# Optimization experiments

Measured on AMD Instinct MI355X. Metric: run time of the kernel, lower is better.

The kernel has to match this reference:

```python
import jax, jax.numpy as jnp
import numpy as np

B, C, T, H, W = 1, 512, 8, 48, 48
GROUPS = 32
EPS = 1e-6


def setup_inputs() -> dict:
    key = jax.random.key(0)
    ks = jax.random.split(key, 6)
    s = 0.02  # init scale for projection weights
    return {
        "x": jax.random.normal(ks[0], (B, C, T, H, W), dtype=jnp.float32),
        "gamma": jnp.ones((C,), dtype=jnp.float32),
        "beta": jnp.zeros((C,), dtype=jnp.float32),
        "wq": jax.random.normal(ks[1], (C, C), dtype=jnp.float32) * s,
        "bq": jnp.zeros((C,), dtype=jnp.float32),
        "wk": jax.random.normal(ks[2], (C, C), dtype=jnp.float32) * s,
        "bk": jnp.zeros((C,), dtype=jnp.float32),
        "wv": jax.random.normal(ks[3], (C, C), dtype=jnp.float32) * s,
        "bv": jnp.zeros((C,), dtype=jnp.float32),
        "wo": jax.random.normal(ks[4], (C, C), dtype=jnp.float32) * s,
        "bo": jnp.zeros((C,), dtype=jnp.float32),
    }


def _group_norm(x, gamma, beta):
    b, c, t, h, w = x.shape
    xg = x.reshape(b, GROUPS, c // GROUPS, t, h, w)
    mu = xg.mean(axis=(2, 3, 4, 5), keepdims=True)
    var = xg.var(axis=(2, 3, 4, 5), keepdims=True)
    xn = ((xg - mu) * jax.lax.rsqrt(var + EPS)).reshape(b, c, t, h, w)
    return xn * gamma[None, :, None, None, None] + beta[None, :, None, None, None]


def _proj(h, wgt, bias):
    # CausalConv3d with kernel_size=1 == pointwise channel linear
    return jnp.einsum('oc,bcthw->bothw', wgt, h) + bias[None, :, None, None, None]


def reference(x, gamma, beta, wq, bq, wk, bk, wv, bv, wo, bo):
    hn = _group_norm(x, gamma, beta)
    q = _proj(hn, wq, bq)
    k = _proj(hn, wk, bk)
    v = _proj(hn, wv, bv)
    b, c, t, h, w = q.shape
    n = h * w
    # per-frame spatial attention: (b, t, n, c)
    qf = q.transpose(0, 2, 3, 4, 1).reshape(b, t, n, c)
    kf = k.transpose(0, 2, 3, 4, 1).reshape(b, t, n, c)
    vf = v.transpose(0, 2, 3, 4, 1).reshape(b, t, n, c)
    scores = jnp.einsum('btqc,btkc->btqk', qf, kf) * (c ** -0.5)
    attn = jax.nn.softmax(scores, axis=-1)
    of = jnp.einsum('btqk,btkc->btqc', attn, vf)
    o = of.reshape(b, t, h, w, c).transpose(0, 4, 1, 2, 3)
    o = _proj(o, wo, bo)
    return x + o
```

## Files before the change

### kernel.cpp

```cpp
#include <hip/hip_runtime.h>
#include <hip/hip_bf16.h>
#include <cstdint>
#include <type_traits>

typedef __attribute__((ext_vector_type(8))) __bf16 bf16x8;
typedef __attribute__((ext_vector_type(4))) float f32x4;
typedef __attribute__((ext_vector_type(2))) long longx2;

struct bf2frag { bf16x8 k0, k1; };

__device__ __forceinline__ float bf2f(unsigned short u) {
  union { uint32_t i; float f; } v; v.i = (uint32_t)u << 16; return v.f;
}
__device__ __forceinline__ unsigned short f2bf(float f) {
  union { float f; uint32_t i; } v{f};
  uint32_t r = v.i + 0x7fffu + ((v.i >> 16) & 1u);
  return (unsigned short)(r >> 16);
}

__device__ __forceinline__ void gll(const void* g, void* l) {
  __builtin_amdgcn_global_load_lds(
      (const __attribute__((address_space(1))) uint32_t*)(uintptr_t)g,
      (__attribute__((address_space(3))) uint32_t*)(uint32_t)(uintptr_t)l,
      16, 0, 0);
}

__device__ __forceinline__ void bar() {
  asm volatile("" ::: "memory");
  __builtin_amdgcn_s_barrier();
  asm volatile("" ::: "memory");
}

#define VMCNT(n) asm volatile("s_waitcnt vmcnt(" #n ")" ::: "memory")

template <int N>
__device__ __forceinline__ void vmw() {
  if constexpr (N == 0) { VMCNT(0); }
  else if constexpr (N == 1) { VMCNT(1); }
  else if constexpr (N == 2) { VMCNT(2); }
  else if constexpr (N == 3) { VMCNT(3); }
  else if constexpr (N == 4) { VMCNT(4); }
  else if constexpr (N == 5) { VMCNT(5); }
  else if constexpr (N == 6) { VMCNT(6); }
  else if constexpr (N == 7) { VMCNT(7); }
  else if constexpr (N == 8) { VMCNT(8); }
  else if constexpr (N == 9) { VMCNT(9); }
  else if constexpr (N == 10) { VMCNT(10); }
  else { VMCNT(12); }
}

__device__ __forceinline__ f32x4 mma(bf16x8 a, bf16x8 b, f32x4 c) {
  return __builtin_amdgcn_mfma_f32_16x16x32_bf16(a, b, c, 0, 0, 0);
}
__device__ __forceinline__ f32x4 mma(long a, long b, f32x4 c) {
  return __builtin_amdgcn_mfma_f32_16x16x32_fp8_fp8(a, b, c, 0, 0, 0);
}
__device__ __forceinline__ f32x4 mmak(const bf2frag& a, const bf2frag& b, f32x4 c, int k2) {
  return k2 ? mma(a.k1, b.k1, c) : mma(a.k0, b.k0, c);
}
__device__ __forceinline__ f32x4 mmak(longx2 a, longx2 b, f32x4 c, int k2) {
  return mma(a[k2], b[k2], c);
}

__device__ __forceinline__ int perm64(int m) {
  return (m & ~63) | (((m >> 3) & 3) << 4) | (((m >> 5) & 1) << 3) | (m & 7);
}

__global__ __launch_bounds__(256) void stats_partial_k(const float* __restrict__ x,
                                                       float* __restrict__ part) {
  const int g = blockIdx.x >> 3, p = blockIdx.x & 7;
  const float* base = x + (long)g * 16 * 18432 + (long)p * 2304;
  float s = 0.f, ss = 0.f;
  for (int idx = threadIdx.x; idx < 16 * 576; idx += 256) {
    const int c = idx / 576, i4 = idx % 576;
    const float4 v = *(const float4*)(base + (long)c * 18432 + i4 * 4);
    s += v.x + v.y + v.z + v.w;
    ss += v.x * v.x + v.y * v.y + v.z * v.z + v.w * v.w;
  }
  __shared__ float rs[256], rss[256];
  rs[threadIdx.x] = s; rss[threadIdx.x] = ss;
  __syncthreads();
  for (int o = 128; o > 0; o >>= 1) {
    if ((int)threadIdx.x < o) { rs[threadIdx.x] += rs[threadIdx.x + o]; rss[threadIdx.x] += rss[threadIdx.x + o]; }
    __syncthreads();
  }
  if (threadIdx.x == 0) { part[blockIdx.x * 2] = rs[0]; part[blockIdx.x * 2 + 1] = rss[0]; }
}

__global__ void stats_final_k(const float* __restrict__ part, float* __restrict__ stats) {
  const int g = threadIdx.x;
  if (g < 32) {
    float s = 0.f, ss = 0.f;
    for (int p = 0; p < 8; ++p) { s += part[(g * 8 + p) * 2]; ss += part[(g * 8 + p) * 2 + 1]; }
    const float mean = s / 294912.0f;
    const float var = ss / 294912.0f - mean * mean;
    stats[g * 2] = mean;
    stats[g * 2 + 1] = rsqrtf(var + 1e-6f);
  }
}

__global__ __launch_bounds__(256) void gn_transpose_k(const float* __restrict__ x,
                                                      const float* __restrict__ stats,
                                                      const float* __restrict__ gamma,
                                                      const float* __restrict__ beta,
                                                      unsigned short* __restrict__ hnT) {
  __shared__ float tile[64][65];
  const int c0 = blockIdx.x * 64, n0 = blockIdx.y * 64;
  const int tn = threadIdx.x & 63, tr = threadIdx.x >> 6;
  for (int cc = tr; cc < 64; cc += 4) {
    const int c = c0 + cc, g = c >> 4;
    const float mean = stats[g * 2], rstd = stats[g * 2 + 1];
    const float v = x[(long)c * 18432 + n0 + tn];
    tile[cc][tn] = (v - mean) * rstd * gamma[c] + beta[c];
  }
  __syncthreads();
  for (int nn = tr; nn < 64; nn += 4) {
    hnT[(long)(n0 + nn) * 512 + c0 + tn] = f2bf(tile[tn][nn]);
  }
}

__global__ __launch_bounds__(256) void pack_bf16_k(const float* __restrict__ w,
                                                   unsigned short* __restrict__ o) {
  const int i = (blockIdx.x * 256 + threadIdx.x) * 4;
  const float4 v = *(const float4*)(w + i);
  ushort4 u; u.x = f2bf(v.x); u.y = f2bf(v.y); u.z = f2bf(v.z); u.w = f2bf(v.w);
  *(ushort4*)(o + i) = u;
}

__global__ void pack_bias_k(const float* __restrict__ bq, const float* __restrict__ bk,
                            float* __restrict__ bqk) {
  const int t = threadIdx.x;
  bqk[t] = (t < 512) ? bq[t] : bk[t - 512];
}

__global__ __launch_bounds__(256) void combine_k(const float* __restrict__ rs,
                                                 float* __restrict__ linv, int ntile) {
  const int row = blockIdx.x * 256 + threadIdx.x;
  const int t = row / 2304, r = row % 2304;
  float L = 0.f;
  for (int x = 0; x < ntile; ++x) L += rs[((long)(t * ntile + x)) * 2304 + r];
  linv[row] = 1.0f / L;
}

template <int BM, int BIAS_MODE, int OUT_MODE, int STATS, int SCALEN, int MODE, int FP8, int P2,
          int WL = 0>
__global__ __launch_bounds__((BM == 256) ? 512 : 256, (WL && FP8) ? 4 : 2)
void gemm256(const void* __restrict__ A, long lda, long sAz,
             const void* __restrict__ B, long ldb, long sBz,
             void* __restrict__ Cp, long ldc, long sCz,
             const float* __restrict__ bias,
             const float* __restrict__ resid,
             float* __restrict__ rowsums,
             const float* __restrict__ linv,
             float alpha, int K, int gx, int gy) {
  constexpr int EB = FP8 ? 1 : 2;
  constexpr int THREADS = (BM == 256) ? 512 : 256;
  constexpr int BN = WL ? 128 : 256;
  constexpr int HBA = (BM / 2) * 64 * EB;
  constexpr int HBB = (BN / 2) * 64 * EB;
  constexpr int GA = HBA / (THREADS * 16);
  constexpr int GB = HBB / (THREADS * 16);
  constexpr int V0 = GB + 2 * GA, V3 = 2 * GB + GA, VP = GB + GA;
  constexpr int NSLOT = WL ? 8 : ((BM == 256) ? 8 : 4);
  constexpr int NSLOTP = NSLOT + 1;
  constexpr int MR = WL ? 4 : 8;
  constexpr int FQ = WL ? 2 : 4;
  constexpr int PRIO = !P2;
  __shared__ alignas(16) unsigned char As[2][2][HBA];
  __shared__ alignas(16) unsigned char Bs[2][2][HBB];
  using ABt2 = typename std::conditional<FP8, longx2, bf2frag>::type;

  const int tid = threadIdx.x;
  const int lane = tid & 63, wid = tid >> 6;
  const int wm = WL ? (wid >> 1) : ((BM == 256) ? (wid & 1) : 0);
  const int wn = WL ? (wid & 1) : ((BM == 256) ? (wid >> 1) : wid);
  int bx, by, bz;
  {
    const int g8 = blockIdx.x & 7, n = blockIdx.x >> 3;
    if (MODE == 0) { bz = g8; bx = n % gx; by = n / gx; }
    else if (MODE == 1) { bz = 0; bx = n % gx; by = g8 * gy + n / gx; }
    else { bz = 0; by = n % gy; bx = g8 * gx + n / gy; }
  }
  const unsigned char* Ab = (const unsigned char*)A + ((long)bz * sAz + (long)bx * BM * lda) * EB;
  const unsigned char* Bb = (const unsigned char*)B + ((long)bz * sBz + (long)by * BN * ldb) * EB;

  auto stageA = [&](int slot, int h, int k0) {
    if constexpr (!FP8) {
      const int ksw = ((tid & 7) << 3) ^ (((tid >> 3) & 7) << 3);
#pragma unroll
      for (int call = 0; call < GA; ++call) {
        const int r = call * (THREADS / 8) + (tid >> 3);
        const int grow = WL ? (((r >> 5) << 6) + h * 32 + (r & 31))
                            : (((r >> 6) << 7) + h * 64 + (r & 63));
        gll(Ab + ((long)grow * lda + k0) * 2 + ksw * 2, &As[slot][h][call * THREADS * 16 + tid * 16]);
      }
    } else {
#pragma unroll
      for (int call = 0; call < GA; ++call) {
        const int l = call * (THREADS / 4) + (tid >> 2);
        const int grow = WL ? (((l >> 5) << 6) + h * 32 + (l & 31))
                            : (((l >> 6) << 7) + h * 64 + (l & 63));
        const int x = (((l & 3) ^ ((l >> 2) & 3)) << 4);
        gll(Ab + (long)grow * lda + k0 + (((tid & 3) << 4) ^ x),
            &As[slot][h][call * THREADS * 16 + tid * 16]);
      }
    }
  };
  auto stageB = [&](int slot, int h, int k0) {
    if constexpr (!FP8) {
      const int ksw = ((tid & 7) << 3) ^ (((tid >> 3) & 7) << 3);
#pragma unroll
      for (int call = 0; call < GB; ++call) {
        const int r = call * (THREADS / 8) + (tid >> 3);
        const int grow = ((r >> 5) << 6) + h * 32 + (r & 31);
        gll(Bb + ((long)grow * ldb + k0) * 2 + ksw * 2, &Bs[slot][h][call * THREADS * 16 + tid * 16]);
      }
    } else {
#pragma unroll
      for (int call = 0; call < GB; ++call) {
        const int l = call * (THREADS / 4) + (tid >> 2);
        const int grow = ((l >> 5) << 6) + h * 32 + (l & 31);
        const int x = (((l & 3) ^ ((l >> 2) & 3)) << 4);
        gll(Bb + (long)grow * ldb + k0 + (((tid & 3) << 4) ^ x),
            &Bs[slot][h][call * THREADS * 16 + tid * 16]);
      }
    }
  };
  auto ldA = [&](int slot, int mh, int fq) -> ABt2 {
    const int r = (WL ? wm * 32 : wm * 64) + fq * 16 + (lane & 15);
    if constexpr (!FP8) {
      bf2frag f;
      const int kk0 = (((lane >> 4) << 3)) ^ ((r & 7) << 3);
      const int kk1 = (32 + ((lane >> 4) << 3)) ^ ((r & 7) << 3);
      f.k0 = *reinterpret_cast<const bf16x8*>(&As[slot][mh][r * 128 + kk0 * 2]);
      f.k1 = *reinterpret_cast<const bf16x8*>(&As[slot][mh][r * 128 + kk1 * 2]);
      return f;
    } else {
      const int x = (((r & 3) ^ ((r >> 2) & 3)) << 4);
      const int kk = ((lane >> 4) << 4) ^ x;
      return *reinterpret_cast<const longx2*>(&As[slot][mh][r * 64 + kk]);
    }
  };
  auto ldB = [&](int slot, int nh, int g) -> ABt2 {
    const int r = wn * 32 + g * 16 + (lane & 15);
    if constexpr (!FP8) {
      bf2frag f;
      const int kk0 = (((lane >> 4) << 3)) ^ ((r & 7) << 3);
      const int kk1 = (32 + ((lane >> 4) << 3)) ^ ((r & 7) << 3);
      f.k0 = *reinterpret_cast<const bf16x8*>(&Bs[slot][nh][r * 128 + kk0 * 2]);
      f.k1 = *reinterpret_cast<const bf16x8*>(&Bs[slot][nh][r * 128 + kk1 * 2]);
      return f;
    } else {
      const int x = (((r & 3) ^ ((r >> 2) & 3)) << 4);
      const int kk = ((lane >> 4) << 4) ^ x;
      return *reinterpret_cast<const longx2*>(&Bs[slot][nh][r * 64 + kk]);
    }
  };

  f32x4 acc[MR][4] = {};
  ABt2 a[4], b0[2], b1[2];

#define READ_A(SLOT, MH)                                                     \
  _Pragma("unroll") for (int fq = 0; fq < FQ; ++fq) a[fq] = ldA(SLOT, MH, fq);
#define READ_B(SLOT, NH, DST)                                                \
  _Pragma("unroll") for (int g = 0; g < 2; ++g) DST[g] = ldB(SLOT, NH, g);
#define MFMA_QUAD(MH, NH, BARR)                                              \
  if constexpr (PRIO) __builtin_amdgcn_s_setprio(1);                         \
  _Pragma("unroll") for (int fq = 0; fq < FQ; ++fq)                          \
    _Pragma("unroll") for (int g = 0; g < 2; ++g)                            \
      _Pragma("unroll") for (int k2 = 0; k2 < 2; ++k2)                       \
        acc[(MH) * FQ + fq][(NH) * 2 + g] =                                  \
            mmak(a[fq], BARR[g], acc[(MH) * FQ + fq][(NH) * 2 + g], k2);     \
  if constexpr (PRIO) __builtin_amdgcn_s_setprio(0);

  const int KT = K >> 6;
  stageB(0, 0, 0);
  stageA(0, 0, 0);
  stageB(0, 1, 0);
  stageA(0, 1, 0);
  stageB(1, 0, 64);
  if constexpr (!P2) stageA(1, 1, 64);
  vmw<VP>();
  bar();

  if constexpr (!P2) {
    for (int W = 0; W < KT; ++W) {
      const int s = W & 1;
      const int kn1 = (W + 1) << 6, kn2 = (W + 2) << 6;
      const bool st1 = (W + 1 < KT), st2 = (W + 2 < KT);
      READ_A(s, 0)
      READ_B(s, 0, b0)
      if (st1) stageA(s ^ 1, 0, kn1);
      bar();
      MFMA_QUAD(0, 0, b0)
      if (st1) { vmw<V0>(); }
      bar();
      READ_B(s, 1, b1)
      if (st1) stageB(s ^ 1, 1, kn1);
      bar();
      MFMA_QUAD(0, 1, b1)
      bar();
      READ_A(s, 1)
      if (st2) stageB(s, 0, kn2);
      bar();
      MFMA_QUAD(1, 1, b1)
      bar();
      if (st2) stageA(s, 1, kn2);
      bar();
      MFMA_QUAD(1, 0, b0)
      if (st2) { vmw<V3>(); } else { vmw<0>(); }
      bar();
    }
  } else {
    for (int W = 0; W < KT; ++W) {
      const int s = W & 1;
      const int kn1 = (W + 1) << 6, kn2 = (W + 2) << 6;
      const bool st1 = (W + 1 < KT), st2 = (W + 2 < KT);
      READ_A(s, 0)
      READ_B(s, 0, b0)
      READ_B(s, 1, b1)
      if (st1) { stageA(s ^ 1, 0, kn1); stageB(s ^ 1, 1, kn1); stageA(s ^ 1, 1, kn1); }
      bar();
      MFMA_QUAD(0, 0, b0)
      MFMA_QUAD(0, 1, b1)
      if (st1) { vmw<2 * (GA + GB)>(); } else { vmw<0>(); }
      bar();
      READ_A(s, 1)
      if (st2) stageB(s, 0, kn2);
      bar();
      MFMA_QUAD(1, 1, b1)
      MFMA_QUAD(1, 0, b0)
      if (st2) { vmw<GA + GB>(); } else if (st1) { vmw<GA>(); } else { vmw<0>(); }
      bar();
    }
  }

  const int mg0 = bx * BM + (WL ? wm * 64 : wm * 128) + ((lane >> 4) << 2);
  const int ng0 = by * BN + wn * 64 + (lane & 15);
  float* red = (float*)&As[0][0][0];
#pragma unroll
  for (int N = 0; N < 4; ++N) {
    const int n = ng0 + (N >> 1) * 32 + (N & 1) * 16;
    const float bn = (BIAS_MODE == 2) ? bias[n] : 0.f;
    const float sc = SCALEN ? linv[(long)bz * 2304 + n] : 1.0f;
    float eN = 0.f;
#pragma unroll
    for (int M = 0; M < MR; ++M) {
      const int m = mg0 + (WL ? ((M >> 1) * 32 + (M & 1) * 16) : ((M >> 2) * 64 + (M & 3) * 16));
      const f32x4 av = acc[M][N];
      float vals[4];
#pragma unroll
      for (int j = 0; j < 4; ++j) {
        vals[j] = av[j] * alpha + ((BIAS_MODE == 1) ? bias[m + j] : bn);
        if (SCALEN) vals[j] *= sc;
        if (STATS) { vals[j] = __expf(vals[j]); eN += vals[j]; }
      }
      if (OUT_MODE == 0) {
        ushort4 o; o.x = f2bf(vals[0]); o.y = f2bf(vals[1]); o.z = f2bf(vals[2]); o.w = f2bf(vals[3]);
        *(ushort4*)((unsigned short*)Cp + (long)bz * sCz + (long)n * ldc + m) = o;
      } else if (OUT_MODE == 2) {
        int pk = __builtin_amdgcn_cvt_pk_fp8_f32(vals[0], vals[1], 0, false);
        pk = __builtin_amdgcn_cvt_pk_fp8_f32(vals[2], vals[3], pk, true);
        *(int*)((unsigned char*)Cp + (long)bz * sCz + (long)n * ldc + perm64(m)) = pk;
      } else {
        const float* rp = resid + (long)n * ldc + m;
        float4 o; o.x = vals[0] + rp[0]; o.y = vals[1] + rp[1]; o.z = vals[2] + rp[2]; o.w = vals[3] + rp[3];
        *(float4*)((float*)Cp + (long)bz * sCz + (long)n * ldc + m) = o;
      }
    }
    if (STATS) {
      const int nloc = wn * 64 + (N >> 1) * 32 + (N & 1) * 16 + (lane & 15);
      const int slot = wm * 4 + (lane >> 4);
      red[nloc * NSLOTP + slot] = eN;
    }
  }
  if (STATS) {
    bar();
    if (tid < BN) {
      float L = 0.f;
#pragma unroll
      for (int s2 = 0; s2 < NSLOT; ++s2) L += red[tid * NSLOTP + s2];
      rowsums[((long)(bz * gx + bx)) * 2304 + by * BN + tid] = L;
    }
  }
#undef READ_A
#undef READ_B
#undef MFMA_QUAD
}

extern "C" void kernel_launch(void* const* d_in, const int* in_sizes, int n_in,
                              void* d_out, int out_size, void* d_ws, size_t ws_size,
                              hipStream_t stream) {
  const float* x = (const float*)d_in[0];
  const float* gamma = (const float*)d_in[1];
  const float* beta = (const float*)d_in[2];
  const float* wq = (const float*)d_in[3];
  const float* bq = (const float*)d_in[4];
  const float* wk = (const float*)d_in[5];
  const float* bk = (const float*)d_in[6];
  const float* wv = (const float*)d_in[7];
  const float* bv = (const float*)d_in[8];
  const float* wo = (const float*)d_in[9];
  const float* bo = (const float*)d_in[10];
  float* out = (float*)d_out;

  char* ws = (char*)d_ws;
  size_t off = 0;
  auto alloc = [&](size_t bytes) {
    char* p = ws + off;
    off = (off + bytes + 255) & ~(size_t)255;
    return p;
  };
  float* part = (float*)alloc(256 * 2 * sizeof(float));
  float* stats = (float*)alloc(32 * 2 * sizeof(float));
  unsigned short* wqkb = (unsigned short*)alloc((size_t)2 * 262144 * 2);
  unsigned short* wvb = (unsigned short*)alloc((size_t)262144 * 2);
  unsigned short* wob = (unsigned short*)alloc((size_t)262144 * 2);
  float* bqk = (float*)alloc(1024 * sizeof(float));
  float* rowsums = (float*)alloc((size_t)8 * 18 * 2304 * sizeof(float));
  float* linv = (float*)alloc((size_t)18432 * sizeof(float));
  unsigned short* hnT = (unsigned short*)alloc((size_t)18432 * 512 * 2);
  unsigned char* qkA = (unsigned char*)alloc((size_t)18432 * 1024);
  unsigned char* vT = (unsigned char*)alloc((size_t)512 * 18432);
  unsigned char* Sm = (unsigned char*)alloc((size_t)8 * 2304 * 2304);
  unsigned short* Ob = hnT;
  (void)ws_size; (void)in_sizes; (void)n_in; (void)out_size;

  stats_partial_k<<<dim3(256), dim3(256), 0, stream>>>(x, part);
  stats_final_k<<<dim3(1), dim3(64), 0, stream>>>(part, stats);
  gn_transpose_k<<<dim3(8, 288), dim3(256), 0, stream>>>(x, stats, gamma, beta, hnT);
  pack_bf16_k<<<dim3(256), dim3(256), 0, stream>>>(wq, wqkb);
  pack_bf16_k<<<dim3(256), dim3(256), 0, stream>>>(wk, wqkb + 262144);
  pack_bf16_k<<<dim3(256), dim3(256), 0, stream>>>(wv, wvb);
  pack_bf16_k<<<dim3(256), dim3(256), 0, stream>>>(wo, wob);
  pack_bias_k<<<dim3(1), dim3(1024), 0, stream>>>(bq, bk, bqk);

  gemm256<128, 1, 2, 0, 0, 1, 0, 1, 1><<<dim3(1152), dim3(256), 0, stream>>>(
      wqkb, 512, 0, hnT, 512, 0, (void*)qkA, 1024, 0, bqk, nullptr, nullptr, nullptr,
      1.0f, 512, 8, 18);
  gemm256<128, 2, 2, 0, 0, 2, 0, 1, 1><<<dim3(576), dim3(256), 0, stream>>>(
      hnT, 512, 0, wvb, 512, 0, (void*)vT, 18432, 0, bv, nullptr, nullptr, nullptr,
      1.0f, 512, 18, 4);
  gemm256<128, 0, 2, 1, 0, 0, 1, 1, 1><<<dim3(2592), dim3(256), 0, stream>>>(
      qkA + 512, 1024, (long)2304 * 1024, qkA, 1024, (long)2304 * 1024, (void*)Sm, 2304,
      (long)2304 * 2304, nullptr, nullptr, rowsums, nullptr,
      0.044194173824159216f, 512, 18, 18);
  combine_k<<<dim3(72), dim3(256), 0, stream>>>(rowsums, linv, 18);
  gemm256<128, 0, 0, 0, 1, 0, 1, 1, 1><<<dim3(576), dim3(256), 0, stream>>>(
      vT, 18432, 2304, Sm, 2304, (long)2304 * 2304, (void*)Ob, 512, (long)2304 * 512,
      nullptr, nullptr, nullptr, linv, 1.0f, 2304, 4, 18);
  gemm256<128, 2, 1, 0, 0, 2, 0, 1, 1><<<dim3(576), dim3(256), 0, stream>>>(
      Ob, 512, 0, wob, 512, 0, (void*)out, 18432, 0, bo, x, nullptr, nullptr,
      1.0f, 512, 18, 4);
}
```

Baseline: 228.3 us.

## Double K-tile depth for fp8 QK^T GEMM and fuse weight pack launches

Adds a KU template parameter that deepens the K step of the fp8 GEMM tile from 64 to 128. Each stage now loads two 64-wide sub-tiles into doubled LDS buffers and runs twice as many MFMAs per barrier round. It is enabled only for the scores GEMM, which has K=512, so there are half as many main-loop iterations and barriers. In exchange LDS use per block doubles and the occupancy hint drops from 4 to 2 blocks per CU. Separately, the four weight-packing launches are merged into one 2D-grid launch to cut launch overhead.

New measurement: 228.2 us. No clear change (-0.0%).

```diff
diff --git a/kernel.cpp b/kernel.cpp
--- a/kernel.cpp
+++ b/kernel.cpp
@@ -119,8 +119,17 @@
   }
 }
 
-__global__ __launch_bounds__(256) void pack_bf16_k(const float* __restrict__ w,
-                                                   unsigned short* __restrict__ o) {
+__global__ __launch_bounds__(256) void pack4_bf16_k(const float* __restrict__ w0,
+                                                    const float* __restrict__ w1,
+                                                    const float* __restrict__ w2,
+                                                    const float* __restrict__ w3,
+                                                    unsigned short* __restrict__ o0,
+                                                    unsigned short* __restrict__ o1,
+                                                    unsigned short* __restrict__ o2,
+                                                    unsigned short* __restrict__ o3) {
+  const int y = blockIdx.y;
+  const float* w = (y == 0) ? w0 : (y == 1) ? w1 : (y == 2) ? w2 : w3;
+  unsigned short* o = (y == 0) ? o0 : (y == 1) ? o1 : (y == 2) ? o2 : o3;
   const int i = (blockIdx.x * 256 + threadIdx.x) * 4;
   const float4 v = *(const float4*)(w + i);
   ushort4 u; u.x = f2bf(v.x); u.y = f2bf(v.y); u.z = f2bf(v.z); u.w = f2bf(v.w);
@@ -143,8 +152,8 @@
 }
 
 template <int BM, int BIAS_MODE, int OUT_MODE, int STATS, int SCALEN, int MODE, int FP8, int P2,
-          int WL = 0>
-__global__ __launch_bounds__((BM == 256) ? 512 : 256, (WL && FP8) ? 4 : 2)
+          int WL = 0, int KU = 1>
+__global__ __launch_bounds__((BM == 256) ? 512 : 256, (WL && FP8) ? (KU == 2 ? 2 : 4) : 2)
 void gemm256(const void* __restrict__ A, long lda, long sAz,
              const void* __restrict__ B, long ldb, long sBz,
              void* __restrict__ Cp, long ldc, long sCz,
@@ -153,13 +162,17 @@
              float* __restrict__ rowsums,
              const float* __restrict__ linv,
              float alpha, int K, int gx, int gy) {
+  static_assert(KU == 1 || FP8, "KU=2 only on fp8 path");
   constexpr int EB = FP8 ? 1 : 2;
   constexpr int THREADS = (BM == 256) ? 512 : 256;
   constexpr int BN = WL ? 128 : 256;
-  constexpr int HBA = (BM / 2) * 64 * EB;
-  constexpr int HBB = (BN / 2) * 64 * EB;
+  constexpr int BK = 64 * KU;
+  constexpr int HBA = (BM / 2) * BK * EB;
+  constexpr int HBB = (BN / 2) * BK * EB;
+  constexpr int HBA0 = HBA / KU, HBB0 = HBB / KU;
   constexpr int GA = HBA / (THREADS * 16);
   constexpr int GB = HBB / (THREADS * 16);
+  constexpr int GA0 = GA / KU, GB0 = GB / KU;
   constexpr int V0 = GB + 2 * GA, V3 = 2 * GB + GA, VP = GB + GA;
   constexpr int NSLOT = WL ? 8 : ((BM == 256) ? 8 : 4);
   constexpr int NSLOTP = NSLOT + 1;
@@ -197,11 +210,12 @@
     } else {
 #pragma unroll
       for (int call = 0; call < GA; ++call) {
-        const int l = call * (THREADS / 4) + (tid >> 2);
+        const int sub = call / GA0, c0 = call % GA0;
+        const int l = c0 * (THREADS / 4) + (tid >> 2);
         const int grow = WL ? (((l >> 5) << 6) + h * 32 + (l & 31))
                             : (((l >> 6) << 7) + h * 64 + (l & 63));
         const int x = (((l & 3) ^ ((l >> 2) & 3)) << 4);
-        gll(Ab + (long)grow * lda + k0 + (((tid & 3) << 4) ^ x),
+        gll(Ab + (long)grow * lda + k0 + sub * 64 + (((tid & 3) << 4) ^ x),
             &As[slot][h][call * THREADS * 16 + tid * 16]);
       }
     }
@@ -218,15 +232,16 @@
     } else {
 #pragma unroll
       for (int call = 0; call < GB; ++call) {
-        const int l = call * (THREADS / 4) + (tid >> 2);
+        const int sub = call / GB0, c0 = call % GB0;
+        const int l = c0 * (THREADS / 4) + (tid >> 2);
         const int grow = ((l >> 5) << 6) + h * 32 + (l & 31);
         const int x = (((l & 3) ^ ((l >> 2) & 3)) << 4);
-        gll(Bb + (long)grow * ldb + k0 + (((tid & 3) << 4) ^ x),
+        gll(Bb + (long)grow * ldb + k0 + sub * 64 + (((tid & 3) << 4) ^ x),
             &Bs[slot][h][call * THREADS * 16 + tid * 16]);
       }
     }
   };
-  auto ldA = [&](int slot, int mh, int fq) -> ABt2 {
+  auto ldA = [&](int slot, int mh, int fq, int sub) -> ABt2 {
     const int r = (WL ? wm * 32 : wm * 64) + fq * 16 + (lane & 15);
     if constexpr (!FP8) {
       bf2frag f;
@@ -238,10 +253,10 @@
     } else {
       const int x = (((r & 3) ^ ((r >> 2) & 3)) << 4);
       const int kk = ((lane >> 4) << 4) ^ x;
-      return *reinterpret_cast<const longx2*>(&As[slot][mh][r * 64 + kk]);
+      return *reinterpret_cast<const longx2*>(&As[slot][mh][sub * HBA0 + r * 64 + kk]);
     }
   };
-  auto ldB = [&](int slot, int nh, int g) -> ABt2 {
+  auto ldB = [&](int slot, int nh, int g, int sub) -> ABt2 {
     const int r = wn * 32 + g * 16 + (lane & 15);
     if constexpr (!FP8) {
       bf2frag f;
@@ -253,40 +268,46 @@
     } else {
       const int x = (((r & 3) ^ ((r >> 2) & 3)) << 4);
       const int kk = ((lane >> 4) << 4) ^ x;
-      return *reinterpret_cast<const longx2*>(&Bs[slot][nh][r * 64 + kk]);
+      return *reinterpret_cast<const longx2*>(&Bs[slot][nh][sub * HBB0 + r * 64 + kk]);
     }
   };
 
   f32x4 acc[MR][4] = {};
-  ABt2 a[4], b0[2], b1[2];
-
-#define READ_A(SLOT, MH)                                                     \
-  _Pragma("unroll") for (int fq = 0; fq < FQ; ++fq) a[fq] = ldA(SLOT, MH, fq);
-#define READ_B(SLOT, NH, DST)                                                \
-  _Pragma("unroll") for (int g = 0; g < 2; ++g) DST[g] = ldB(SLOT, NH, g);
-#define MFMA_QUAD(MH, NH, BARR)                                              \
-  if constexpr (PRIO) __builtin_amdgcn_s_setprio(1);                         \
-  _Pragma("unroll") for (int fq = 0; fq < FQ; ++fq)                          \
-    _Pragma("unroll") for (int g = 0; g < 2; ++g)                            \
-      _Pragma("unroll") for (int k2 = 0; k2 < 2; ++k2)                       \
-        acc[(MH) * FQ + fq][(NH) * 2 + g] =                                  \
-            mmak(a[fq], BARR[g], acc[(MH) * FQ + fq][(NH) * 2 + g], k2);     \
+  ABt2 a[FQ * KU], b0[2 * KU], b1[2 * KU];
+
+#define READ_A(SLOT, MH)                                                       \
+  _Pragma("unroll") for (int fq = 0; fq < FQ; ++fq)                            \
+    _Pragma("unroll") for (int sub = 0; sub < KU; ++sub)                       \
+      a[fq * KU + sub] = ldA(SLOT, MH, fq, sub);
+#define READ_B(SLOT, NH, DST)                                                  \
+  _Pragma("unroll") for (int g = 0; g < 2; ++g)                                \
+    _Pragma("unroll") for (int sub = 0; sub < KU; ++sub)                       \
+      DST[g * KU + sub] = ldB(SLOT, NH, g, sub);
+#define MFMA_QUAD(MH, NH, BARR)                                                \
+  if constexpr (PRIO) __builtin_amdgcn_s_setprio(1);                           \
+  _Pragma("unroll") for (int fq = 0; fq < FQ; ++fq)                            \
+    _Pragma("unroll") for (int g = 0; g < 2; ++g)                              \
+      _Pragma("unroll") for (int sub = 0; sub < KU; ++sub)                     \
+        _Pragma("unroll") for (int k2 = 0; k2 < 2; ++k2)                       \
+          acc[(MH) * FQ + fq][(NH) * 2 + g] =                                  \
+              mmak(a[fq * KU + sub], BARR[g * KU + sub],                       \
+                   acc[(MH) * FQ + fq][(NH) * 2 + g], k2);                     \
   if constexpr (PRIO) __builtin_amdgcn_s_setprio(0);
 
-  const int KT = K >> 6;
+  const int KT = K / BK;
   stageB(0, 0, 0);
   stageA(0, 0, 0);
   stageB(0, 1, 0);
   stageA(0, 1, 0);
-  stageB(1, 0, 64);
-  if constexpr (!P2) stageA(1, 1, 64);
+  stageB(1, 0, BK);
+  if constexpr (!P2) stageA(1, 1, BK);
   vmw<VP>();
   bar();
 
   if constexpr (!P2) {
     for (int W = 0; W < KT; ++W) {
       const int s = W & 1;
-      const int kn1 = (W + 1) << 6, kn2 = (W + 2) << 6;
+      const int kn1 = (W + 1) * BK, kn2 = (W + 2) * BK;
       const bool st1 = (W + 1 < KT), st2 = (W + 2 < KT);
       READ_A(s, 0)
       READ_B(s, 0, b0)
@@ -314,7 +335,7 @@
   } else {
     for (int W = 0; W < KT; ++W) {
       const int s = W & 1;
-      const int kn1 = (W + 1) << 6, kn2 = (W + 2) << 6;
+      const int kn1 = (W + 1) * BK, kn2 = (W + 2) * BK;
       const bool st1 = (W + 1 < KT), st2 = (W + 2 < KT);
       READ_A(s, 0)
       READ_B(s, 0, b0)
@@ -429,10 +450,8 @@
   stats_partial_k<<<dim3(256), dim3(256), 0, stream>>>(x, part);
   stats_final_k<<<dim3(1), dim3(64), 0, stream>>>(part, stats);
   gn_transpose_k<<<dim3(8, 288), dim3(256), 0, stream>>>(x, stats, gamma, beta, hnT);
-  pack_bf16_k<<<dim3(256), dim3(256), 0, stream>>>(wq, wqkb);
-  pack_bf16_k<<<dim3(256), dim3(256), 0, stream>>>(wk, wqkb + 262144);
-  pack_bf16_k<<<dim3(256), dim3(256), 0, stream>>>(wv, wvb);
-  pack_bf16_k<<<dim3(256), dim3(256), 0, stream>>>(wo, wob);
+  pack4_bf16_k<<<dim3(256, 4), dim3(256), 0, stream>>>(wq, wk, wv, wo,
+                                                       wqkb, wqkb + 262144, wvb, wob);
   pack_bias_k<<<dim3(1), dim3(1024), 0, stream>>>(bq, bk, bqk);
 
   gemm256<128, 1, 2, 0, 0, 1, 0, 1, 1><<<dim3(1152), dim3(256), 0, stream>>>(
@@ -441,7 +460,7 @@
   gemm256<128, 2, 2, 0, 0, 2, 0, 1, 1><<<dim3(576), dim3(256), 0, stream>>>(
       hnT, 512, 0, wvb, 512, 0, (void*)vT, 18432, 0, bv, nullptr, nullptr, nullptr,
       1.0f, 512, 18, 4);
-  gemm256<128, 0, 2, 1, 0, 0, 1, 1, 1><<<dim3(2592), dim3(256), 0, stream>>>(
+  gemm256<128, 0, 2, 1, 0, 0, 1, 1, 1, 2><<<dim3(2592), dim3(256), 0, stream>>>(
       qkA + 512, 1024, (long)2304 * 1024, qkA, 1024, (long)2304 * 1024, (void*)Sm, 2304,
       (long)2304 * 2304, nullptr, nullptr, rowsums, nullptr,
       0.044194173824159216f, 512, 18, 18);
```
